# Kernel optimization log

Measured on AMD Instinct MI355X. Metric: run time of the kernel, lower is better.

Reference implementation:

```python
import jax, jax.numpy as jnp
import numpy as np

NUM_HEADS = 12
QUAD_C = 5.0

def setup_inputs() -> dict:
    key = jax.random.key(0)
    k1, k2, k3 = jax.random.split(key, 3)
    B, N, C = 8, 1024, 768
    x = jax.random.normal(k1, (B, N, C), dtype=jnp.float32)
    qkv_w = jax.random.normal(k2, (3 * C, C), dtype=jnp.float32) * (C ** -0.5)
    proj_w = jax.random.normal(k3, (C, C), dtype=jnp.float32) * (C ** -0.5)
    proj_b = jnp.zeros((C,), dtype=jnp.float32)
    return {"x": x, "qkv_w": qkv_w, "proj_w": proj_w, "proj_b": proj_b}

def reference(x, qkv_w, proj_w, proj_b):
    B, N, C = x.shape
    H = NUM_HEADS
    hd = C // H
    scale = hd ** -0.5
    # qkv projection: [B,N,3C] -> [3,B,H,N,hd]
    qkv = (x @ qkv_w.T).reshape(B, N, 3, H, hd).transpose(2, 0, 3, 1, 4)
    q, k, v = qkv[0], qkv[1], qkv[2]
    # explicit N x N attention scores
    attn = jnp.einsum('bhnd,bhmd->bhnm', q, k) * scale
    # Quad2 normalization: square(x + c) / row-sum
    t = jnp.square(attn + QUAD_C)
    attn = t / jnp.sum(t, axis=-1, keepdims=True)
    out = jnp.einsum('bhnm,bhmd->bhnd', attn, v)  # [B,H,N,hd]
    out = out.transpose(0, 2, 1, 3).reshape(B, N, C)
    return out @ proj_w.T + proj_b
```

## Files before the change

kernel.cpp:

```cpp
#include <hip/hip_runtime.h>
#include <hip/hip_bf16.h>
#include <stdint.h>


typedef short  s8v  __attribute__((ext_vector_type(8)));
typedef float  f4v  __attribute__((ext_vector_type(4)));

__device__ inline uint16_t f2bf(float f) {
    union { float f; uint32_t u; } c; c.f = f;
    uint32_t u = c.u;
    u += 0x7fffu + ((u >> 16) & 1u);
    return (uint16_t)(u >> 16);
}
__device__ inline uint32_t pack2bf(float a, float b) {
    union { __hip_bfloat162 v; uint32_t u; } c;
    c.v = __float22bfloat162_rn(float2{a, b});
    return c.u;
}

__device__ inline void cp16(const uint16_t* g, uint16_t* l) {
    __builtin_amdgcn_global_load_lds(
        (const __attribute__((address_space(1))) void*)g,
        (__attribute__((address_space(3))) void*)l, 16, 0, 0);
}

__global__ __launch_bounds__(256) void cvt_all(
    const float* __restrict__ x, const float* __restrict__ qw,
    const float* __restrict__ pw, uint16_t* __restrict__ dst)
{
    int i = blockIdx.x * 256 + threadIdx.x;
    if (i >= 1081344) return;
    const float* s;
    if (i < 786432)       s = x  + (size_t)i * 8;
    else if (i < 1007616) s = qw + ((size_t)i - 786432) * 8;
    else                  s = pw + ((size_t)i - 1007616) * 8;
    const float4* sp = reinterpret_cast<const float4*>(s);
    float4 a = sp[0], b = sp[1];
    s8v o;
    o[0] = (short)f2bf(a.x); o[1] = (short)f2bf(a.y);
    o[2] = (short)f2bf(a.z); o[3] = (short)f2bf(a.w);
    o[4] = (short)f2bf(b.x); o[5] = (short)f2bf(b.y);
    o[6] = (short)f2bf(b.z); o[7] = (short)f2bf(b.w);
    *reinterpret_cast<s8v*>(dst + (size_t)i * 8) = o;
}

template <int EPI>
__global__ __launch_bounds__(256) void gemm_bt(
    const uint16_t* __restrict__ A, const uint16_t* __restrict__ Bm,
    uint16_t* __restrict__ qb, uint16_t* __restrict__ kb, uint16_t* __restrict__ vb,
    const float* __restrict__ bias, float* __restrict__ Cout, int K)
{
    __shared__ uint16_t Al[128 * 32];
    __shared__ uint16_t Bl[128 * 32];

    const int tid  = threadIdx.x;
    const int wave = tid >> 6, lane = tid & 63;
    const int quad = lane >> 4, l16 = lane & 15;
    const int wM = wave >> 1, wN = wave & 1;
    const int bM = blockIdx.x, bN = blockIdx.y;

    f4v acc[4][4];
#pragma unroll
    for (int i = 0; i < 4; i++)
#pragma unroll
        for (int j = 0; j < 4; j++) { f4v z = {0.f, 0.f, 0.f, 0.f}; acc[i][j] = z; }

    const uint16_t* Ag = A  + (size_t)bM * 128 * K;
    const uint16_t* Bg = Bm + (size_t)bN * 128 * K;

    const int e0 = tid * 8;
    const int r0 = e0 >> 5, c0 = e0 & 31;

    for (int kc = 0; kc < K; kc += 32) {
        __syncthreads();
        cp16(Ag + (size_t)r0 * K + kc + c0,        &Al[e0]);
        cp16(Ag + (size_t)(r0 + 64) * K + kc + c0, &Al[e0 + 2048]);
        cp16(Bg + (size_t)r0 * K + kc + c0,        &Bl[e0]);
        cp16(Bg + (size_t)(r0 + 64) * K + kc + c0, &Bl[e0 + 2048]);
        __syncthreads();

        s8v af[4], bf[4];
#pragma unroll
        for (int t = 0; t < 4; t++) {
            af[t] = *reinterpret_cast<const s8v*>(&Al[(wM * 64 + t * 16 + l16) * 32 + quad * 8]);
            bf[t] = *reinterpret_cast<const s8v*>(&Bl[(wN * 64 + t * 16 + l16) * 32 + quad * 8]);
        }
#pragma unroll
        for (int tm = 0; tm < 4; tm++)
#pragma unroll
            for (int tn = 0; tn < 4; tn++)
                acc[tm][tn] = __builtin_amdgcn_mfma_f32_16x16x32_bf16(af[tm], bf[tn], acc[tm][tn], 0, 0, 0);
    }

#pragma unroll
    for (int tm = 0; tm < 4; tm++) {
#pragma unroll
        for (int tn = 0; tn < 4; tn++) {
            const int col = bN * 128 + wN * 64 + tn * 16 + l16;
            if (EPI == 0) {
                const int three = col / 768;
                const int rem   = col - three * 768;
                const int h = rem >> 6, d = rem & 63;
                const int n0 = bM * 128 + wM * 64 + tm * 16 + quad * 4;
                const int b = n0 >> 10, n = n0 & 1023;
                if (three == 2) {
                    ushort4 pk;
                    pk.x = f2bf(acc[tm][tn][0]);
                    pk.y = f2bf(acc[tm][tn][1]);
                    pk.z = f2bf(acc[tm][tn][2]);
                    pk.w = f2bf(acc[tm][tn][3]);
                    *reinterpret_cast<ushort4*>(
                        &vb[((size_t)((b * 12 + h) * 64 + d)) * 1024 + n]) = pk;
                } else {
                    uint16_t* dst = (three == 0) ? qb : kb;
#pragma unroll
                    for (int reg = 0; reg < 4; reg++)
                        dst[((size_t)((b * 12 + h) * 1024 + n + reg)) * 64 + d] =
                            f2bf(acc[tm][tn][reg]);
                }
            } else {
#pragma unroll
                for (int reg = 0; reg < 4; reg++) {
                    const int row = bM * 128 + wM * 64 + tm * 16 + quad * 4 + reg;
                    Cout[(size_t)row * 768 + col] = acc[tm][tn][reg] + bias[col];
                }
            }
        }
    }
}

__global__ __launch_bounds__(128, 2) void attn_quad(
    const uint16_t* __restrict__ Q, const uint16_t* __restrict__ K,
    const uint16_t* __restrict__ VT, uint16_t* __restrict__ O)
{
    const int qt = blockIdx.x;
    const int bh = blockIdx.y;
    const int b = bh / 12, h = bh - (bh / 12) * 12;
    const uint16_t* Qp = Q  + (size_t)bh * 65536;
    const uint16_t* Kp = K  + (size_t)bh * 65536;
    const uint16_t* Vp = VT + (size_t)bh * 65536;

    const int tid  = threadIdx.x;
    const int wave = tid >> 6, lane = tid & 63;
    const int quad = lane >> 4, l16 = lane & 15;

    __shared__ uint16_t Kl[64 * 64];
    __shared__ uint16_t Vl[64 * 64];
    __shared__ uint16_t Pl[2][16][80];

    s8v qf[4][2];
#pragma unroll
    for (int s = 0; s < 4; s++) {
        const uint16_t* qp = Qp + (size_t)(qt * 128 + wave * 64 + s * 16 + l16) * 64 + quad * 8;
        qf[s][0] = *reinterpret_cast<const s8v*>(qp);
        qf[s][1] = *reinterpret_cast<const s8v*>(qp + 32);
    }

    s8v ones;
#pragma unroll
    for (int i = 0; i < 8; i++) ones[i] = (short)0x3F80;

    f4v U[4][4], U5[4];
#pragma unroll
    for (int s = 0; s < 4; s++) {
        f4v z = {0.f, 0.f, 0.f, 0.f};
        U5[s] = z;
#pragma unroll
        for (int c = 0; c < 4; c++) U[s][c] = z;
    }

    for (int mt = 0; mt < 16; mt++) {
        __syncthreads();
#pragma unroll
        for (int r = 0; r < 4; r++) {
            const int e   = (tid + r * 128) * 8;
            const int row = e >> 6;
            const int cl  = ((e >> 3) & 7) ^ (row & 7);
            cp16(Kp + (size_t)mt * 4096 + (size_t)row * 64 + cl * 8, &Kl[e]);
            cp16(Vp + (size_t)row * 1024 + mt * 64 + cl * 8, &Vl[e]);
        }
        __syncthreads();

        s8v kf[4][2], vf[4][2];
#pragma unroll
        for (int c = 0; c < 4; c++) {
            const int rr = c * 16 + l16;
#pragma unroll
            for (int kk = 0; kk < 2; kk++) {
                const int pc = (kk * 4 + quad) ^ (rr & 7);
                kf[c][kk] = *reinterpret_cast<const s8v*>(&Kl[rr * 64 + (pc << 3)]);
                vf[c][kk] = *reinterpret_cast<const s8v*>(&Vl[rr * 64 + (pc << 3)]);
            }
        }

#pragma unroll
        for (int s = 0; s < 4; s++) {
            f4v st[4];
#pragma unroll
            for (int cm = 0; cm < 4; cm++) {
                f4v z = {0.f, 0.f, 0.f, 0.f};
                z = __builtin_amdgcn_mfma_f32_16x16x32_bf16(kf[cm][0], qf[s][0], z, 0, 0, 0);
                z = __builtin_amdgcn_mfma_f32_16x16x32_bf16(kf[cm][1], qf[s][1], z, 0, 0, 0);
                st[cm] = z;
            }
#pragma unroll
            for (int cm = 0; cm < 4; cm++) {
                float t0 = st[cm][0] * 0.125f + 5.0f; t0 *= t0;
                float t1 = st[cm][1] * 0.125f + 5.0f; t1 *= t1;
                float t2 = st[cm][2] * 0.125f + 5.0f; t2 *= t2;
                float t3 = st[cm][3] * 0.125f + 5.0f; t3 *= t3;
                uint2 pk; pk.x = pack2bf(t0, t1); pk.y = pack2bf(t2, t3);
                *reinterpret_cast<uint2*>(&Pl[wave][l16][cm * 16 + quad * 4]) = pk;
            }
#pragma unroll
            for (int kc = 0; kc < 2; kc++) {
                s8v pf = *reinterpret_cast<const s8v*>(&Pl[wave][l16][kc * 32 + quad * 8]);
                U5[s] = __builtin_amdgcn_mfma_f32_16x16x32_bf16(pf, ones, U5[s], 0, 0, 0);
#pragma unroll
                for (int cd = 0; cd < 4; cd++)
                    U[s][cd] = __builtin_amdgcn_mfma_f32_16x16x32_bf16(pf, vf[cd][kc], U[s][cd], 0, 0, 0);
            }
        }
    }

#pragma unroll
    for (int s = 0; s < 4; s++) {
        float inv[4];
#pragma unroll
        for (int reg = 0; reg < 4; reg++) inv[reg] = 1.0f / U5[s][reg];
#pragma unroll
        for (int cd = 0; cd < 4; cd++) {
#pragma unroll
            for (int reg = 0; reg < 4; reg++) {
                const int n = qt * 128 + wave * 64 + s * 16 + quad * 4 + reg;
                const int d = cd * 16 + l16;
                O[((size_t)(b * 1024 + n)) * 768 + h * 64 + d] = f2bf(U[s][cd][reg] * inv[reg]);
            }
        }
    }
}

extern "C" void kernel_launch(void* const* d_in, const int* in_sizes, int n_in,
                              void* d_out, int out_size, void* d_ws, size_t ws_size,
                              hipStream_t stream)
{
    const float* x      = (const float*)d_in[0];
    const float* qkv_w  = (const float*)d_in[1];
    const float* proj_w = (const float*)d_in[2];
    const float* proj_b = (const float*)d_in[3];
    float* out = (float*)d_out;

    const size_t NEL = (size_t)8 * 1024 * 768;
    uint16_t* xb  = (uint16_t*)d_ws;
    uint16_t* qwb = xb  + NEL;
    uint16_t* pwb = qwb + 1769472;
    uint16_t* qb  = pwb + 589824;
    uint16_t* kb  = qb  + NEL;
    uint16_t* vb  = kb  + NEL;
    uint16_t* ao  = vb  + NEL;

    cvt_all<<<4224, 256, 0, stream>>>(x, qkv_w, proj_w, xb);

    gemm_bt<0><<<dim3(64, 18), 256, 0, stream>>>(xb, qwb, qb, kb, vb, nullptr, nullptr, 768);
    attn_quad<<<dim3(8, 96), 128, 0, stream>>>(qb, kb, vb, ao);
    gemm_bt<1><<<dim3(64, 6), 256, 0, stream>>>(ao, pwb, nullptr, nullptr, nullptr, proj_b, out, 768);
}
```

Before: 198.6 us.

## Pipeline GEMMs with triple-buffered LDS, larger tiles, swizzle and XCD block remap

```diff
diff --git a/kernel.cpp b/kernel.cpp
--- a/kernel.cpp
+++ b/kernel.cpp
@@ -45,19 +45,25 @@
 }
 
 template <int EPI>
-__global__ __launch_bounds__(256) void gemm_bt(
+__global__ __launch_bounds__(512, 2) void gemm_pipe(
     const uint16_t* __restrict__ A, const uint16_t* __restrict__ Bm,
     uint16_t* __restrict__ qb, uint16_t* __restrict__ kb, uint16_t* __restrict__ vb,
-    const float* __restrict__ bias, float* __restrict__ Cout, int K)
+    const float* __restrict__ bias, float* __restrict__ Cout, int K, int GN)
 {
-    __shared__ uint16_t Al[128 * 32];
-    __shared__ uint16_t Bl[128 * 32];
+    __shared__ uint16_t Al[3][128 * 64];
+    __shared__ uint16_t Bl[3][256 * 64];
 
     const int tid  = threadIdx.x;
     const int wave = tid >> 6, lane = tid & 63;
     const int quad = lane >> 4, l16 = lane & 15;
-    const int wM = wave >> 1, wN = wave & 1;
-    const int bM = blockIdx.x, bN = blockIdx.y;
+    const int wM = wave >> 2, wN = wave & 3;
+
+    const int nwg = (int)gridDim.x;
+    const int wg  = ((int)blockIdx.x & 7) * (nwg >> 3) + ((int)blockIdx.x >> 3);
+    const int bM = wg / GN, bN = wg - bM * GN;
+
+    const uint16_t* Ag = A  + (size_t)bM * 128 * K;
+    const uint16_t* Bg = Bm + (size_t)bN * 256 * K;
 
     f4v acc[4][4];
 #pragma unroll
@@ -65,38 +71,77 @@
 #pragma unroll
         for (int j = 0; j < 4; j++) { f4v z = {0.f, 0.f, 0.f, 0.f}; acc[i][j] = z; }
 
-    const uint16_t* Ag = A  + (size_t)bM * 128 * K;
-    const uint16_t* Bg = Bm + (size_t)bN * 128 * K;
-
-    const int e0 = tid * 8;
-    const int r0 = e0 >> 5, c0 = e0 & 31;
-
-    for (int kc = 0; kc < K; kc += 32) {
-        __syncthreads();
-        cp16(Ag + (size_t)r0 * K + kc + c0,        &Al[e0]);
-        cp16(Ag + (size_t)(r0 + 64) * K + kc + c0, &Al[e0 + 2048]);
-        cp16(Bg + (size_t)r0 * K + kc + c0,        &Bl[e0]);
-        cp16(Bg + (size_t)(r0 + 64) * K + kc + c0, &Bl[e0 + 2048]);
-        __syncthreads();
-
-        s8v af[4], bf[4];
-#pragma unroll
-        for (int t = 0; t < 4; t++) {
-            af[t] = *reinterpret_cast<const s8v*>(&Al[(wM * 64 + t * 16 + l16) * 32 + quad * 8]);
-            bf[t] = *reinterpret_cast<const s8v*>(&Bl[(wN * 64 + t * 16 + l16) * 32 + quad * 8]);
-        }
-#pragma unroll
-        for (int tm = 0; tm < 4; tm++)
-#pragma unroll
-            for (int tn = 0; tn < 4; tn++)
-                acc[tm][tn] = __builtin_amdgcn_mfma_f32_16x16x32_bf16(af[tm], bf[tn], acc[tm][tn], 0, 0, 0);
-    }
+    const int nt = K >> 6;
+
+    auto stage = [&](int t, int slot) {
+        const int kc = t << 6;
+        uint16_t* as = &Al[slot][0];
+        uint16_t* bs = &Bl[slot][0];
+#pragma unroll
+        for (int u = 0; u < 2; ++u) {
+            const int ch = tid + u * 512;
+            const int r  = ch >> 3, lc = (ch & 7) ^ (r & 7);
+            cp16(Ag + (size_t)r * K + kc + lc * 8, as + ch * 8);
+        }
+#pragma unroll
+        for (int u = 0; u < 4; ++u) {
+            const int ch = tid + u * 512;
+            const int r  = ch >> 3, lc = (ch & 7) ^ (r & 7);
+            cp16(Bg + (size_t)r * K + kc + lc * 8, bs + ch * 8);
+        }
+    };
+
+    auto compute = [&](int slot) {
+        const uint16_t* as = &Al[slot][0];
+        const uint16_t* bs = &Bl[slot][0];
+        s8v af[4][2], bfr[4][2];
+#pragma unroll
+        for (int x = 0; x < 4; ++x) {
+            const int ra = wM * 64 + x * 16 + l16;
+            const int rb = wN * 64 + x * 16 + l16;
+#pragma unroll
+            for (int kk = 0; kk < 2; ++kk) {
+                const int pa = (kk * 4 + quad) ^ (ra & 7);
+                const int pb = (kk * 4 + quad) ^ (rb & 7);
+                af[x][kk]  = *reinterpret_cast<const s8v*>(as + ra * 64 + pa * 8);
+                bfr[x][kk] = *reinterpret_cast<const s8v*>(bs + rb * 64 + pb * 8);
+            }
+        }
+        __builtin_amdgcn_s_setprio(1);
+#pragma unroll
+        for (int kk = 0; kk < 2; ++kk)
+#pragma unroll
+            for (int tm = 0; tm < 4; ++tm)
+#pragma unroll
+                for (int tn = 0; tn < 4; ++tn)
+                    acc[tm][tn] = __builtin_amdgcn_mfma_f32_16x16x32_bf16(
+                        af[tm][kk], bfr[tn][kk], acc[tm][tn], 0, 0, 0);
+        __builtin_amdgcn_s_setprio(0);
+    };
+
+    stage(0, 0);
+    stage(1, 1);
+
+    int cs = 0;
+    for (int t = 0; t < nt - 1; ++t) {
+        asm volatile("s_waitcnt vmcnt(6)" ::: "memory");
+        __builtin_amdgcn_s_barrier();
+        if (t + 2 < nt) {
+            int ss = cs + 2; if (ss >= 3) ss -= 3;
+            stage(t + 2, ss);
+        }
+        compute(cs);
+        cs = (cs == 2) ? 0 : cs + 1;
+    }
+    asm volatile("s_waitcnt vmcnt(0)" ::: "memory");
+    __builtin_amdgcn_s_barrier();
+    compute(cs);
 
 #pragma unroll
     for (int tm = 0; tm < 4; tm++) {
 #pragma unroll
         for (int tn = 0; tn < 4; tn++) {
-            const int col = bN * 128 + wN * 64 + tn * 16 + l16;
+            const int col = bN * 256 + wN * 64 + tn * 16 + l16;
             if (EPI == 0) {
                 const int three = col / 768;
                 const int rem   = col - three * 768;
@@ -261,7 +306,7 @@
 
     cvt_all<<<4224, 256, 0, stream>>>(x, qkv_w, proj_w, xb);
 
-    gemm_bt<0><<<dim3(64, 18), 256, 0, stream>>>(xb, qwb, qb, kb, vb, nullptr, nullptr, 768);
+    gemm_pipe<0><<<576, 512, 0, stream>>>(xb, qwb, qb, kb, vb, nullptr, nullptr, 768, 9);
     attn_quad<<<dim3(8, 96), 128, 0, stream>>>(qb, kb, vb, ao);
-    gemm_bt<1><<<dim3(64, 6), 256, 0, stream>>>(ao, pwb, nullptr, nullptr, nullptr, proj_b, out, 768);
-}
+    gemm_pipe<1><<<192, 512, 0, stream>>>(ao, pwb, nullptr, nullptr, nullptr, proj_b, out, 768, 3);
+}
```

Measured after the change: 202.6 us. 1.02x slower.

## Widen GEMM K-tile to 64 with XOR-swizzled LDS and remapped block order

Applied to the files above, without the earlier changes.

```diff
diff --git a/kernel.cpp b/kernel.cpp
--- a/kernel.cpp
+++ b/kernel.cpp
@@ -45,51 +45,72 @@
 }
 
 template <int EPI>
-__global__ __launch_bounds__(256) void gemm_bt(
+__global__ __launch_bounds__(256) void gemm_m97(
     const uint16_t* __restrict__ A, const uint16_t* __restrict__ Bm,
     uint16_t* __restrict__ qb, uint16_t* __restrict__ kb, uint16_t* __restrict__ vb,
-    const float* __restrict__ bias, float* __restrict__ Cout, int K)
-{
-    __shared__ uint16_t Al[128 * 32];
-    __shared__ uint16_t Bl[128 * 32];
+    const float* __restrict__ bias, float* __restrict__ Cout, int GN)
+{
+    constexpr int K  = 768;
+    constexpr int NT = K / 64;
+
+    __shared__ uint16_t Al[128 * 64];
+    __shared__ uint16_t Bl[128 * 64];
 
     const int tid  = threadIdx.x;
     const int wave = tid >> 6, lane = tid & 63;
     const int quad = lane >> 4, l16 = lane & 15;
     const int wM = wave >> 1, wN = wave & 1;
-    const int bM = blockIdx.x, bN = blockIdx.y;
-
-    f4v acc[4][4];
-#pragma unroll
-    for (int i = 0; i < 4; i++)
-#pragma unroll
-        for (int j = 0; j < 4; j++) { f4v z = {0.f, 0.f, 0.f, 0.f}; acc[i][j] = z; }
+
+    const int nwg = (int)gridDim.x;
+    const int wg  = ((int)blockIdx.x & 7) * (nwg >> 3) + ((int)blockIdx.x >> 3);
+    const int bM = wg / GN, bN = wg - bM * GN;
 
     const uint16_t* Ag = A  + (size_t)bM * 128 * K;
     const uint16_t* Bg = Bm + (size_t)bN * 128 * K;
 
-    const int e0 = tid * 8;
-    const int r0 = e0 >> 5, c0 = e0 & 31;
-
-    for (int kc = 0; kc < K; kc += 32) {
-        __syncthreads();
-        cp16(Ag + (size_t)r0 * K + kc + c0,        &Al[e0]);
-        cp16(Ag + (size_t)(r0 + 64) * K + kc + c0, &Al[e0 + 2048]);
-        cp16(Bg + (size_t)r0 * K + kc + c0,        &Bl[e0]);
-        cp16(Bg + (size_t)(r0 + 64) * K + kc + c0, &Bl[e0 + 2048]);
-        __syncthreads();
-
-        s8v af[4], bf[4];
-#pragma unroll
-        for (int t = 0; t < 4; t++) {
-            af[t] = *reinterpret_cast<const s8v*>(&Al[(wM * 64 + t * 16 + l16) * 32 + quad * 8]);
-            bf[t] = *reinterpret_cast<const s8v*>(&Bl[(wN * 64 + t * 16 + l16) * 32 + quad * 8]);
-        }
-#pragma unroll
-        for (int tm = 0; tm < 4; tm++)
-#pragma unroll
-            for (int tn = 0; tn < 4; tn++)
-                acc[tm][tn] = __builtin_amdgcn_mfma_f32_16x16x32_bf16(af[tm], bf[tn], acc[tm][tn], 0, 0, 0);
+    f4v acc[4][4];
+#pragma unroll
+    for (int i = 0; i < 4; i++)
+#pragma unroll
+        for (int j = 0; j < 4; j++) { f4v z = {0.f, 0.f, 0.f, 0.f}; acc[i][j] = z; }
+
+    for (int t = 0; t < NT; ++t) {
+        __syncthreads();
+#pragma unroll
+        for (int u = 0; u < 4; ++u) {
+            const int ch = tid + u * 256;
+            const int r  = ch >> 3, lc = (ch & 7) ^ (r & 7);
+            cp16(Ag + (size_t)r * K + t * 64 + lc * 8, &Al[ch * 8]);
+        }
+#pragma unroll
+        for (int u = 0; u < 4; ++u) {
+            const int ch = tid + u * 256;
+            const int r  = ch >> 3, lc = (ch & 7) ^ (r & 7);
+            cp16(Bg + (size_t)r * K + t * 64 + lc * 8, &Bl[ch * 8]);
+        }
+        __syncthreads();
+
+        s8v af[4][2], bq[4][2];
+#pragma unroll
+        for (int x = 0; x < 4; ++x) {
+            const int ra = wM * 64 + x * 16 + l16;
+            const int rb = wN * 64 + x * 16 + l16;
+#pragma unroll
+            for (int kk = 0; kk < 2; ++kk) {
+                const int pa = (kk * 4 + quad) ^ (ra & 7);
+                const int pb = (kk * 4 + quad) ^ (rb & 7);
+                af[x][kk] = *reinterpret_cast<const s8v*>(&Al[ra * 64 + pa * 8]);
+                bq[x][kk] = *reinterpret_cast<const s8v*>(&Bl[rb * 64 + pb * 8]);
+            }
+        }
+#pragma unroll
+        for (int kk = 0; kk < 2; ++kk)
+#pragma unroll
+            for (int tm = 0; tm < 4; ++tm)
+#pragma unroll
+                for (int tn = 0; tn < 4; ++tn)
+                    acc[tm][tn] = __builtin_amdgcn_mfma_f32_16x16x32_bf16(
+                        af[tm][kk], bq[tn][kk], acc[tm][tn], 0, 0, 0);
     }
 
 #pragma unroll
@@ -261,7 +282,7 @@
 
     cvt_all<<<4224, 256, 0, stream>>>(x, qkv_w, proj_w, xb);
 
-    gemm_bt<0><<<dim3(64, 18), 256, 0, stream>>>(xb, qwb, qb, kb, vb, nullptr, nullptr, 768);
+    gemm_m97<0><<<1152, 256, 0, stream>>>(xb, qwb, qb, kb, vb, nullptr, nullptr, 18);
     attn_quad<<<dim3(8, 96), 128, 0, stream>>>(qb, kb, vb, ao);
-    gemm_bt<1><<<dim3(64, 6), 256, 0, stream>>>(ao, pwb, nullptr, nullptr, nullptr, proj_b, out, 768);
-}
+    gemm_m97<1><<<384, 256, 0, stream>>>(ao, pwb, nullptr, nullptr, nullptr, proj_b, out, 6);
+}
```

After: 185.9 us (median of 2 runs). -6.4%, faster.
